# Optimization experiments

Measured on AMD Instinct MI355X. Metric: run time of the kernel, lower is better.

The kernel has to match this reference:

```python
import jax, jax.numpy as jnp
import numpy as np

H = 128          # hidden_dim
L = 3            # n_layers
G = 128          # num graphs in batch
BN_EPS = 1e-5


def setup_inputs() -> dict:
    key = jax.random.key(0)
    ks = jax.random.split(key, 16)
    N, E, ND, ED = 2048, 8192, 32, 16
    s = lambda k, shape, fan: jax.random.normal(k, shape, dtype=jnp.float32) / np.sqrt(fan)
    return {
        "x": jax.random.normal(ks[0], (N, ND), dtype=jnp.float32),
        "edge_index": jax.random.randint(ks[1], (2, E), 0, N),
        "edge_attr": jax.random.normal(ks[2], (E, ED), dtype=jnp.float32),
        "batch": jnp.sort(jax.random.randint(ks[3], (N,), 0, G)),
        "node_W": s(ks[4], (ND, H), ND),
        "node_b": jnp.zeros((H,), jnp.float32),
        "edge_W": s(ks[5], (L, ED, H * H), ED),
        "edge_b": jnp.zeros((L, H * H), jnp.float32),
        "root_W": s(ks[6], (L, H, H), H),
        "conv_bias": jnp.zeros((L, H), jnp.float32),
        "bn_gamma": jnp.ones((L, H), jnp.float32),
        "bn_beta": jnp.zeros((L, H), jnp.float32),
        "cls_W1": s(ks[7], (H, 64), H),
        "cls_b1": jnp.zeros((64,), jnp.float32),
        "cls_W2": s(ks[8], (64, 1), 64),
        "cls_b2": jnp.zeros((1,), jnp.float32),
    }


def _segment_mean(vals, ids, num_segments):
    ssum = jax.ops.segment_sum(vals, ids, num_segments=num_segments)
    cnt = jax.ops.segment_sum(jnp.ones((vals.shape[0],), vals.dtype), ids,
                              num_segments=num_segments)
    return ssum / jnp.maximum(cnt, 1.0)[:, None]


def reference(x, edge_index, edge_attr, batch, node_W, node_b, edge_W, edge_b,
              root_W, conv_bias, bn_gamma, bn_beta, cls_W1, cls_b1, cls_W2, cls_b2):
    N = x.shape[0]
    src, dst = edge_index[0], edge_index[1]
    h = x @ node_W + node_b                                   # [N, H]
    for l in range(L):
        # edge-conditioned weights: [E, H, H]
        W = (edge_attr @ edge_W[l] + edge_b[l]).reshape(-1, H, H)
        msg = jnp.einsum('ei,eio->eo', h[src], W)             # gather + per-edge matmul
        agg = _segment_mean(msg, dst, N)                      # scatter-mean
        x_new = h @ root_W[l] + agg + conv_bias[l]
        # BatchNorm (batch statistics, training-mode math)
        mu = jnp.mean(x_new, axis=0)
        var = jnp.var(x_new, axis=0)
        x_new = (x_new - mu) * jax.lax.rsqrt(var + BN_EPS) * bn_gamma[l] + bn_beta[l]
        x_new = jax.nn.relu(x_new)                            # dropout omitted (eval)
        h = h + x_new                                         # residual
    g = _segment_mean(h, batch, G)                            # global mean pool [G, H]
    out = jax.nn.relu(g @ cls_W1 + cls_b1) @ cls_W2 + cls_b2  # classifier
    return out.squeeze(-1)                                    # [G]
```

## Files before the change

### kernel.cpp

```cpp
#include <hip/hip_runtime.h>
#include <cstddef>
#include <cstdint>

#define H 128
#define EDIM 16
#define NLAYER 3
#define NSLICE 18
#define WCOLS (NSLICE * H)
#define PCOLS (EDIM * H)

typedef unsigned short ushort_t;
typedef unsigned int uint_t;
typedef __attribute__((ext_vector_type(8))) short bf16x8;
typedef __attribute__((ext_vector_type(4))) float f32x4;

__device__ __forceinline__ ushort_t f2bf(float f) {
    uint_t u = __builtin_bit_cast(uint_t, f);
    u += 0x7fffu + ((u >> 16) & 1u);
    return (ushort_t)(u >> 16);
}
__device__ __forceinline__ float bf_lo(uint_t u) {
    return __builtin_bit_cast(float, u << 16);
}
__device__ __forceinline__ float bf_hi(uint_t u) {
    return __builtin_bit_cast(float, u & 0xffff0000u);
}

__global__ __launch_bounds__(256) void setup_kernel(
    const int* __restrict__ dst, const int* __restrict__ batch,
    int* __restrict__ histD, float* __restrict__ cntG, int E, int N,
    const float* __restrict__ eW, const float* __restrict__ eb,
    const float* __restrict__ rW, ushort_t* __restrict__ Wt,
    const float* __restrict__ x, const float* __restrict__ nW,
    const float* __restrict__ nbias, float* __restrict__ h,
    ushort_t* __restrict__ hbf)
{
    __shared__ alignas(16) ushort_t tile[128][136];
    const int t = threadIdx.x;

    if (blockIdx.x < 32) {
        const int g = blockIdx.x * 256 + t;
        if (g < E) atomicAdd(&histD[dst[g]], 1);
        if (g < N) atomicAdd(&cntG[batch[g]], 1.f);
        return;
    }

    if (blockIdx.x < 86) {
        const int b = blockIdx.x - 32;
        const int l = b / NSLICE, s = b % NSLICE;
        const float* S = (s < 16) ? (eW + ((size_t)l * 16 + s) * (H * H))
                       : (s == 16 ? (eb + (size_t)l * H * H)
                                  : (rW + (size_t)l * H * H));
        const int k = t >> 1, o0 = (t & 1) * 64;
#pragma unroll
        for (int j = 0; j < 64; j += 4) {
            float4 v = *(const float4*)&S[(size_t)k * H + o0 + j];
            tile[k][o0 + j + 0] = f2bf(v.x);
            tile[k][o0 + j + 1] = f2bf(v.y);
            tile[k][o0 + j + 2] = f2bf(v.z);
            tile[k][o0 + j + 3] = f2bf(v.w);
        }
        __syncthreads();
        const int n = t >> 1, k0 = (t & 1) * 64;
        ushort_t* outp = Wt + ((size_t)l * WCOLS + s * H + n) * H + k0;
#pragma unroll 8
        for (int j = 0; j < 64; ++j) outp[j] = tile[k0 + j][n];
        return;
    }

    const int b2 = blockIdx.x - 86;
    const int bm = (b2 >> 1) * 64;
    const int bn = (b2 & 1) * 64;
    float (*As)[68] = (float (*)[68])(void*)tile;
    float (*Bs)[68] = ((float (*)[68])(void*)tile) + 16;

    const int tx = t & 15, ty = t >> 4;
    float acc[4][4];
#pragma unroll
    for (int i = 0; i < 4; ++i)
#pragma unroll
        for (int j = 0; j < 4; ++j) acc[i][j] = 0.f;

    const int ka = t & 15, ma = t >> 4;
    const int nb2 = t & 63, kb = t >> 6;

    for (int k0 = 0; k0 < 32; k0 += 16) {
#pragma unroll
        for (int r = 0; r < 4; ++r)
            As[ka][ma + 16 * r] = x[(size_t)(bm + ma + 16 * r) * 32 + k0 + ka];
#pragma unroll
        for (int r = 0; r < 4; ++r)
            Bs[kb + 4 * r][nb2] = nW[(size_t)(k0 + kb + 4 * r) * H + bn + nb2];
        __syncthreads();
#pragma unroll
        for (int kk = 0; kk < 16; ++kk) {
            const float4 a4 = *(const float4*)&As[kk][ty * 4];
            const float4 b4 = *(const float4*)&Bs[kk][tx * 4];
            const float a[4] = {a4.x, a4.y, a4.z, a4.w};
            const float b[4] = {b4.x, b4.y, b4.z, b4.w};
#pragma unroll
            for (int i = 0; i < 4; ++i)
#pragma unroll
                for (int j = 0; j < 4; ++j)
                    acc[i][j] = fmaf(a[i], b[j], acc[i][j]);
        }
        __syncthreads();
    }

#pragma unroll
    for (int i = 0; i < 4; ++i) {
        const int row = bm + ty * 4 + i;
        float4 v;
        v.x = acc[i][0] + nbias[bn + tx * 4 + 0];
        v.y = acc[i][1] + nbias[bn + tx * 4 + 1];
        v.z = acc[i][2] + nbias[bn + tx * 4 + 2];
        v.w = acc[i][3] + nbias[bn + tx * 4 + 3];
        *(float4*)&h[(size_t)row * H + bn + tx * 4] = v;
        ushort_t* o = &hbf[(size_t)row * H + bn + tx * 4];
        o[0] = f2bf(v.x); o[1] = f2bf(v.y); o[2] = f2bf(v.z); o[3] = f2bf(v.w);
    }
}

__global__ __launch_bounds__(256) void mfma_gemm(
    const ushort_t* __restrict__ hbf, const ushort_t* __restrict__ Wt,
    ushort_t* __restrict__ Pb, float* __restrict__ QR)
{
    __shared__ ushort_t As[64][136];
    __shared__ ushort_t Bs[64][136];
    const int tid = threadIdx.x;
    const int v0 = blockIdx.y * 64;
    const int n0 = blockIdx.x * 64;

    {
        const int row = tid >> 2, col0 = (tid & 3) * 32;
        const ushort_t* ga = hbf + (size_t)(v0 + row) * H + col0;
        const ushort_t* gb = Wt + (size_t)(n0 + row) * H + col0;
#pragma unroll
        for (int j = 0; j < 32; j += 8) {
            *(uint4*)&As[row][col0 + j] = *(const uint4*)(ga + j);
            *(uint4*)&Bs[row][col0 + j] = *(const uint4*)(gb + j);
        }
    }
    __syncthreads();

    const int wave = tid >> 6, lane = tid & 63;
    const int l15 = lane & 15, kg = lane >> 4;
    const int mrow = wave * 16 + l15;

    f32x4 acc0 = {0.f, 0.f, 0.f, 0.f};
    f32x4 acc1 = {0.f, 0.f, 0.f, 0.f};
    f32x4 acc2 = {0.f, 0.f, 0.f, 0.f};
    f32x4 acc3 = {0.f, 0.f, 0.f, 0.f};

#pragma unroll
    for (int s = 0; s < 4; ++s) {
        const int k = s * 32 + kg * 8;
        bf16x8 a = *(const bf16x8*)&As[mrow][k];
        bf16x8 b0 = *(const bf16x8*)&Bs[0 * 16 + l15][k];
        bf16x8 b1 = *(const bf16x8*)&Bs[1 * 16 + l15][k];
        bf16x8 b2 = *(const bf16x8*)&Bs[2 * 16 + l15][k];
        bf16x8 b3 = *(const bf16x8*)&Bs[3 * 16 + l15][k];
        acc0 = __builtin_amdgcn_mfma_f32_16x16x32_bf16(a, b0, acc0, 0, 0, 0);
        acc1 = __builtin_amdgcn_mfma_f32_16x16x32_bf16(a, b1, acc1, 0, 0, 0);
        acc2 = __builtin_amdgcn_mfma_f32_16x16x32_bf16(a, b2, acc2, 0, 0, 0);
        acc3 = __builtin_amdgcn_mfma_f32_16x16x32_bf16(a, b3, acc3, 0, 0, 0);
    }

    const int slice = n0 >> 7;
    const int lo = n0 & 127;
    const int row0 = v0 + wave * 16 + kg * 4;
    if (slice < 16) {
        ushort_t* op = Pb + (size_t)row0 * PCOLS + slice * H + lo + l15;
#pragma unroll
        for (int r = 0; r < 4; ++r) {
            op[(size_t)r * PCOLS + 0]  = f2bf(acc0[r]);
            op[(size_t)r * PCOLS + 16] = f2bf(acc1[r]);
            op[(size_t)r * PCOLS + 32] = f2bf(acc2[r]);
            op[(size_t)r * PCOLS + 48] = f2bf(acc3[r]);
        }
    } else {
        float* op = QR + (size_t)row0 * 256 + (slice - 16) * H + lo + l15;
#pragma unroll
        for (int r = 0; r < 4; ++r) {
            op[(size_t)r * 256 + 0]  = acc0[r];
            op[(size_t)r * 256 + 16] = acc1[r];
            op[(size_t)r * 256 + 32] = acc2[r];
            op[(size_t)r * 256 + 48] = acc3[r];
        }
    }
}

__global__ __launch_bounds__(256) void edge_msg(
    const ushort_t* __restrict__ Pb, const float* __restrict__ QR,
    const float* __restrict__ ea, const int* __restrict__ srcArr,
    const int* __restrict__ dstArr, float* __restrict__ agg, int E)
{
    const int wave = threadIdx.x >> 6, lane = threadIdx.x & 63;
    const int e = blockIdx.x * 4 + wave;
    if (e >= E) return;
    const int s  = srcArr[e];
    const int dv = dstArr[e];
    const float* eap = ea + (size_t)e * EDIM;
    const float4 w0 = *(const float4*)(eap + 0);
    const float4 w1 = *(const float4*)(eap + 4);
    const float4 w2 = *(const float4*)(eap + 8);
    const float4 w3 = *(const float4*)(eap + 12);
    const float w[16] = {w0.x, w0.y, w0.z, w0.w, w1.x, w1.y, w1.z, w1.w,
                         w2.x, w2.y, w2.z, w2.w, w3.x, w3.y, w3.z, w3.w};
    const uint_t* prow = (const uint_t*)Pb + (size_t)s * (PCOLS / 2) + lane;
    const float2 q2 = *(const float2*)(QR + (size_t)s * 256 + 2 * lane);
    float m0 = q2.x, m1 = q2.y;
#pragma unroll
    for (int d = 0; d < EDIM; ++d) {
        const uint_t u = prow[(size_t)d * 64];
        m0 = fmaf(w[d], bf_lo(u), m0);
        m1 = fmaf(w[d], bf_hi(u), m1);
    }
    atomicAdd(&agg[(size_t)dv * H + 2 * lane], m0);
    atomicAdd(&agg[(size_t)dv * H + 2 * lane + 1], m1);
}

__global__ __launch_bounds__(256) void node_stats(
    float* __restrict__ agg, const float* __restrict__ QR,
    const int* __restrict__ histD, const float* __restrict__ conv_b,
    float* __restrict__ xnew, float* __restrict__ bnS, float* __restrict__ bnQ)
{
    __shared__ float sS[H];
    __shared__ float sQ[H];
    const int tid = threadIdx.x;
    const int c = tid & 127, half = tid >> 7;
    const int v0 = blockIdx.x * 8 + half * 4;
    const float cb = conv_b[c];
    float s = 0.f, q = 0.f;
#pragma unroll
    for (int j = 0; j < 4; ++j) {
        const int v = v0 + j;
        const int deg = histD[v];
        const float rc = 1.0f / (float)(deg > 0 ? deg : 1);
        const size_t ix = (size_t)v * H + c;
        const float val = agg[ix] * rc + QR[(size_t)v * 256 + H + c] + cb;
        xnew[ix] = val;
        agg[ix] = 0.f;
        s += val;
        q += val * val;
    }
    if (half == 0) { sS[c] = s; sQ[c] = q; }
    __syncthreads();
    if (half == 1) {
        atomicAdd(&bnS[c], sS[c] + s);
        atomicAdd(&bnQ[c], sQ[c] + q);
    }
}

__global__ __launch_bounds__(256) void bn_apply(
    float* __restrict__ h, ushort_t* __restrict__ hbf,
    const float* __restrict__ xnew,
    const float* __restrict__ bnS, const float* __restrict__ bnQ,
    const float* __restrict__ gamma, const float* __restrict__ beta,
    const int* __restrict__ batch, float* __restrict__ gsum, int N, int last)
{
    const int idx = blockIdx.x * 256 + threadIdx.x;
    const int c = idx & 127;
    const int v = idx >> 7;
    const float invN = 1.0f / (float)N;
    const float mu = bnS[c] * invN;
    const float var = bnQ[c] * invN - mu * mu;
    const float val = (xnew[idx] - mu) * rsqrtf(var + 1e-5f) * gamma[c] + beta[c];
    const float hn = h[idx] + fmaxf(val, 0.f);
    h[idx] = hn;
    hbf[idx] = f2bf(hn);
    if (last) atomicAdd(&gsum[batch[v] * H + c], hn);
}

__global__ void classifier_kernel(
    const float* __restrict__ gsum, const float* __restrict__ cntG,
    const float* __restrict__ W1, const float* __restrict__ b1,
    const float* __restrict__ W2, const float* __restrict__ b2,
    float* __restrict__ out)
{
    const int g = blockIdx.x;
    const int j = threadIdx.x;
    const float rc = 1.0f / fmaxf(cntG[g], 1.0f);
    float acc = b1[j];
#pragma unroll 8
    for (int i = 0; i < H; ++i)
        acc = fmaf(gsum[g * H + i] * rc, W1[i * 64 + j], acc);
    float pv = fmaxf(acc, 0.f) * W2[j];
#pragma unroll
    for (int off = 32; off > 0; off >>= 1)
        pv += __shfl_down(pv, off);
    if (j == 0) out[g] = pv + b2[0];
}

extern "C" void kernel_launch(void* const* d_in, const int* in_sizes, int n_in,
                              void* d_out, int out_size, void* d_ws, size_t ws_size,
                              hipStream_t stream)
{
    const float* x      = (const float*)d_in[0];
    const int*   eidx   = (const int*)  d_in[1];
    const float* eattr  = (const float*)d_in[2];
    const int*   batch  = (const int*)  d_in[3];
    const float* node_W = (const float*)d_in[4];
    const float* node_b = (const float*)d_in[5];
    const float* edge_W = (const float*)d_in[6];
    const float* edge_b = (const float*)d_in[7];
    const float* root_W = (const float*)d_in[8];
    const float* conv_b = (const float*)d_in[9];
    const float* gamma  = (const float*)d_in[10];
    const float* beta   = (const float*)d_in[11];
    const float* W1     = (const float*)d_in[12];
    const float* b1     = (const float*)d_in[13];
    const float* W2     = (const float*)d_in[14];
    const float* b2     = (const float*)d_in[15];
    float* out = (float*)d_out;

    const int N = in_sizes[0] / 32;
    const int E = in_sizes[1] / 2;
    const int G = out_size;

    int* histD  = (int*)d_ws;
    float* cntG = (float*)(histD + N);
    float* bnS  = cntG + G;
    float* bnQ  = bnS + NLAYER * H;
    float* gsum = bnQ + NLAYER * H;
    float* agg  = gsum + (size_t)G * H;
    float* h    = agg + (size_t)N * H;
    float* xnew = h + (size_t)N * H;
    ushort_t* hbf = (ushort_t*)(xnew + (size_t)N * H);
    ushort_t* Wt  = hbf + (size_t)N * H;
    ushort_t* Pb  = Wt + (size_t)NLAYER * WCOLS * H;
    float* QR   = (float*)(Pb + (size_t)N * PCOLS);

    const size_t zbytes = ((size_t)N + G + 2 * NLAYER * H
                         + (size_t)G * H + (size_t)N * H) * 4;
    hipMemsetAsync(d_ws, 0, zbytes, stream);

    const int* src = eidx;
    const int* dst = eidx + E;

    setup_kernel<<<150, 256, 0, stream>>>(
        dst, batch, histD, cntG, E, N, edge_W, edge_b, root_W, Wt,
        x, node_W, node_b, h, hbf);

    for (int l = 0; l < NLAYER; ++l) {
        mfma_gemm<<<dim3(WCOLS / 64, N / 64), 256, 0, stream>>>(
            hbf, Wt + (size_t)l * WCOLS * H, Pb, QR);
        edge_msg<<<(E + 3) / 4, 256, 0, stream>>>(
            Pb, QR, eattr, src, dst, agg, E);
        node_stats<<<N / 8, 256, 0, stream>>>(
            agg, QR, histD, conv_b + (size_t)l * H,
            xnew, bnS + l * H, bnQ + l * H);
        bn_apply<<<(N * H) / 256, 256, 0, stream>>>(
            h, hbf, xnew, bnS + l * H, bnQ + l * H,
            gamma + (size_t)l * H, beta + (size_t)l * H,
            batch, gsum, N, l == NLAYER - 1);
    }

    classifier_kernel<<<G, 64, 0, stream>>>(gsum, cntG, W1, b1, W2, b2, out);
}
```

Measured before the change: 198.9 us.

## Fuse BatchNorm apply into next layer GEMM and final pooling into classifier

Removes the separate bn_apply kernel. Each layer's GEMM now recomputes the BN scale and shift, applies residual plus ReLU while loading its A tile, and converts to bf16 in place. Only the first column block writes the new fp32 h to a ping-pong buffer. The last layer's BN, residual and mean pooling move into the classifier, which reads contiguous node ranges per graph (relying on batch being sorted) instead of using atomics. This saves three launches and a full pass over the node features each layer, at the cost of redundant BN/ReLU work across all 36 column blocks and a serial prefix sum over cntG in each classifier block.

```diff
diff --git a/kernel.cpp b/kernel.cpp
--- a/kernel.cpp
+++ b/kernel.cpp
@@ -32,8 +32,7 @@
     const float* __restrict__ eW, const float* __restrict__ eb,
     const float* __restrict__ rW, ushort_t* __restrict__ Wt,
     const float* __restrict__ x, const float* __restrict__ nW,
-    const float* __restrict__ nbias, float* __restrict__ h,
-    ushort_t* __restrict__ hbf)
+    const float* __restrict__ nbias, float* __restrict__ hA)
 {
     __shared__ alignas(16) ushort_t tile[128][136];
     const int t = threadIdx.x;
@@ -106,7 +105,6 @@
         }
         __syncthreads();
     }
-
 #pragma unroll
     for (int i = 0; i < 4; ++i) {
         const int row = bm + ty * 4 + i;
@@ -115,30 +113,75 @@
         v.y = acc[i][1] + nbias[bn + tx * 4 + 1];
         v.z = acc[i][2] + nbias[bn + tx * 4 + 2];
         v.w = acc[i][3] + nbias[bn + tx * 4 + 3];
-        *(float4*)&h[(size_t)row * H + bn + tx * 4] = v;
-        ushort_t* o = &hbf[(size_t)row * H + bn + tx * 4];
-        o[0] = f2bf(v.x); o[1] = f2bf(v.y); o[2] = f2bf(v.z); o[3] = f2bf(v.w);
+        *(float4*)&hA[(size_t)row * H + bn + tx * 4] = v;
     }
 }
 
 __global__ __launch_bounds__(256) void mfma_gemm(
-    const ushort_t* __restrict__ hbf, const ushort_t* __restrict__ Wt,
-    ushort_t* __restrict__ Pb, float* __restrict__ QR)
+    const float* __restrict__ hsrc, const float* __restrict__ xnew,
+    float* __restrict__ hdst, const ushort_t* __restrict__ Wt,
+    ushort_t* __restrict__ Pb, float* __restrict__ QR,
+    const float* __restrict__ bnS, const float* __restrict__ bnQ,
+    const float* __restrict__ gamma, const float* __restrict__ beta,
+    int N, int fuse)
 {
     __shared__ ushort_t As[64][136];
     __shared__ ushort_t Bs[64][136];
+    __shared__ float sc[H], sh[H];
     const int tid = threadIdx.x;
+    const int n0 = blockIdx.x * 64;
     const int v0 = blockIdx.y * 64;
-    const int n0 = blockIdx.x * 64;
-
+
+    if (fuse) {
+        if (tid < H) {
+            const float invN = 1.0f / (float)N;
+            const float mu = bnS[tid] * invN;
+            const float var = bnQ[tid] * invN - mu * mu;
+            const float s_ = rsqrtf(var + 1e-5f) * gamma[tid];
+            sc[tid] = s_;
+            sh[tid] = beta[tid] - mu * s_;
+        }
+        __syncthreads();
+    }
+
+    const int row = tid >> 2, col0 = (tid & 3) * 32;
     {
-        const int row = tid >> 2, col0 = (tid & 3) * 32;
-        const ushort_t* ga = hbf + (size_t)(v0 + row) * H + col0;
         const ushort_t* gb = Wt + (size_t)(n0 + row) * H + col0;
 #pragma unroll
-        for (int j = 0; j < 32; j += 8) {
-            *(uint4*)&As[row][col0 + j] = *(const uint4*)(ga + j);
-            *(uint4*)&Bs[row][col0 + j] = *(const uint4*)(gb + j);
+        for (int jj = 0; jj < 32; jj += 8)
+            *(uint4*)&Bs[row][col0 + jj] = *(const uint4*)(gb + jj);
+    }
+    {
+        const float* ga = hsrc + (size_t)(v0 + row) * H + col0;
+        if (!fuse) {
+#pragma unroll
+            for (int jj = 0; jj < 32; jj += 4) {
+                const float4 v = *(const float4*)(ga + jj);
+                uint2 u;
+                u.x = (uint_t)f2bf(v.x) | ((uint_t)f2bf(v.y) << 16);
+                u.y = (uint_t)f2bf(v.z) | ((uint_t)f2bf(v.w) << 16);
+                *(uint2*)&As[row][col0 + jj] = u;
+            }
+        } else {
+            const float* gx = xnew + (size_t)(v0 + row) * H + col0;
+            float* gh = hdst + (size_t)(v0 + row) * H + col0;
+#pragma unroll
+            for (int jj = 0; jj < 32; jj += 4) {
+                const float4 hv = *(const float4*)(ga + jj);
+                const float4 xv = *(const float4*)(gx + jj);
+                const float4 scv = *(const float4*)&sc[col0 + jj];
+                const float4 shv = *(const float4*)&sh[col0 + jj];
+                float4 hn;
+                hn.x = hv.x + fmaxf(xv.x * scv.x + shv.x, 0.f);
+                hn.y = hv.y + fmaxf(xv.y * scv.y + shv.y, 0.f);
+                hn.z = hv.z + fmaxf(xv.z * scv.z + shv.z, 0.f);
+                hn.w = hv.w + fmaxf(xv.w * scv.w + shv.w, 0.f);
+                if (blockIdx.x == 0) *(float4*)(gh + jj) = hn;
+                uint2 u;
+                u.x = (uint_t)f2bf(hn.x) | ((uint_t)f2bf(hn.y) << 16);
+                u.y = (uint_t)f2bf(hn.z) | ((uint_t)f2bf(hn.w) << 16);
+                *(uint2*)&As[row][col0 + jj] = u;
+            }
         }
     }
     __syncthreads();
@@ -146,16 +189,14 @@
     const int wave = tid >> 6, lane = tid & 63;
     const int l15 = lane & 15, kg = lane >> 4;
     const int mrow = wave * 16 + l15;
-
     f32x4 acc0 = {0.f, 0.f, 0.f, 0.f};
     f32x4 acc1 = {0.f, 0.f, 0.f, 0.f};
     f32x4 acc2 = {0.f, 0.f, 0.f, 0.f};
     f32x4 acc3 = {0.f, 0.f, 0.f, 0.f};
-
-#pragma unroll
-    for (int s = 0; s < 4; ++s) {
-        const int k = s * 32 + kg * 8;
-        bf16x8 a = *(const bf16x8*)&As[mrow][k];
+#pragma unroll
+    for (int s2 = 0; s2 < 4; ++s2) {
+        const int k = s2 * 32 + kg * 8;
+        bf16x8 a  = *(const bf16x8*)&As[mrow][k];
         bf16x8 b0 = *(const bf16x8*)&Bs[0 * 16 + l15][k];
         bf16x8 b1 = *(const bf16x8*)&Bs[1 * 16 + l15][k];
         bf16x8 b2 = *(const bf16x8*)&Bs[2 * 16 + l15][k];
@@ -165,7 +206,6 @@
         acc2 = __builtin_amdgcn_mfma_f32_16x16x32_bf16(a, b2, acc2, 0, 0, 0);
         acc3 = __builtin_amdgcn_mfma_f32_16x16x32_bf16(a, b3, acc3, 0, 0, 0);
     }
-
     const int slice = n0 >> 7;
     const int lo = n0 & 127;
     const int row0 = v0 + wave * 16 + kg * 4;
@@ -252,44 +292,51 @@
     }
 }
 
-__global__ __launch_bounds__(256) void bn_apply(
-    float* __restrict__ h, ushort_t* __restrict__ hbf,
-    const float* __restrict__ xnew,
+__global__ __launch_bounds__(256) void classifier_kernel(
+    const float* __restrict__ h2, const float* __restrict__ xnew,
     const float* __restrict__ bnS, const float* __restrict__ bnQ,
     const float* __restrict__ gamma, const float* __restrict__ beta,
-    const int* __restrict__ batch, float* __restrict__ gsum, int N, int last)
-{
-    const int idx = blockIdx.x * 256 + threadIdx.x;
-    const int c = idx & 127;
-    const int v = idx >> 7;
-    const float invN = 1.0f / (float)N;
-    const float mu = bnS[c] * invN;
-    const float var = bnQ[c] * invN - mu * mu;
-    const float val = (xnew[idx] - mu) * rsqrtf(var + 1e-5f) * gamma[c] + beta[c];
-    const float hn = h[idx] + fmaxf(val, 0.f);
-    h[idx] = hn;
-    hbf[idx] = f2bf(hn);
-    if (last) atomicAdd(&gsum[batch[v] * H + c], hn);
-}
-
-__global__ void classifier_kernel(
-    const float* __restrict__ gsum, const float* __restrict__ cntG,
+    const float* __restrict__ cntG,
     const float* __restrict__ W1, const float* __restrict__ b1,
     const float* __restrict__ W2, const float* __restrict__ b2,
-    float* __restrict__ out)
-{
+    float* __restrict__ out, int N)
+{
+    __shared__ float sc[H], sh[H], part[H], pooled[H];
     const int g = blockIdx.x;
-    const int j = threadIdx.x;
-    const float rc = 1.0f / fmaxf(cntG[g], 1.0f);
-    float acc = b1[j];
+    const int tid = threadIdx.x;
+    const int c = tid & 127, half = tid >> 7;
+    if (tid < H) {
+        const float invN = 1.0f / (float)N;
+        const float mu = bnS[tid] * invN;
+        const float var = bnQ[tid] * invN - mu * mu;
+        const float s_ = rsqrtf(var + 1e-5f) * gamma[tid];
+        sc[tid] = s_;
+        sh[tid] = beta[tid] - mu * s_;
+    }
+    __syncthreads();
+    int lo = 0;
+    for (int i = 0; i < g; ++i) lo += (int)cntG[i];
+    const int cnt = (int)cntG[g];
+    float s = 0.f;
+    for (int v = lo + half; v < lo + cnt; v += 2) {
+        const size_t ix = (size_t)v * H + c;
+        s += h2[ix] + fmaxf(xnew[ix] * sc[c] + sh[c], 0.f);
+    }
+    if (half == 0) part[c] = s;
+    __syncthreads();
+    if (half == 1) pooled[c] = (part[c] + s) / fmaxf((float)cnt, 1.0f);
+    __syncthreads();
+    if (tid < 64) {
+        float acc = b1[tid];
 #pragma unroll 8
-    for (int i = 0; i < H; ++i)
-        acc = fmaf(gsum[g * H + i] * rc, W1[i * 64 + j], acc);
-    float pv = fmaxf(acc, 0.f) * W2[j];
-#pragma unroll
-    for (int off = 32; off > 0; off >>= 1)
-        pv += __shfl_down(pv, off);
-    if (j == 0) out[g] = pv + b2[0];
+        for (int i = 0; i < H; ++i)
+            acc = fmaf(pooled[i], W1[i * 64 + tid], acc);
+        float pv = fmaxf(acc, 0.f) * W2[tid];
+#pragma unroll
+        for (int off = 32; off > 0; off >>= 1)
+            pv += __shfl_down(pv, off);
+        if (tid == 0) out[g] = pv + b2[0];
+    }
 }
 
 extern "C" void kernel_launch(void* const* d_in, const int* in_sizes, int n_in,
@@ -322,17 +369,15 @@
     float* cntG = (float*)(histD + N);
     float* bnS  = cntG + G;
     float* bnQ  = bnS + NLAYER * H;
-    float* gsum = bnQ + NLAYER * H;
-    float* agg  = gsum + (size_t)G * H;
-    float* h    = agg + (size_t)N * H;
-    float* xnew = h + (size_t)N * H;
-    ushort_t* hbf = (ushort_t*)(xnew + (size_t)N * H);
-    ushort_t* Wt  = hbf + (size_t)N * H;
-    ushort_t* Pb  = Wt + (size_t)NLAYER * WCOLS * H;
+    float* agg  = bnQ + NLAYER * H;
+    float* hA   = agg + (size_t)N * H;
+    float* hB   = hA + (size_t)N * H;
+    float* xnew = hB + (size_t)N * H;
+    ushort_t* Wt = (ushort_t*)(xnew + (size_t)N * H);
+    ushort_t* Pb = Wt + (size_t)NLAYER * WCOLS * H;
     float* QR   = (float*)(Pb + (size_t)N * PCOLS);
 
-    const size_t zbytes = ((size_t)N + G + 2 * NLAYER * H
-                         + (size_t)G * H + (size_t)N * H) * 4;
+    const size_t zbytes = ((size_t)N + G + 2 * NLAYER * H + (size_t)N * H) * 4;
     hipMemsetAsync(d_ws, 0, zbytes, stream);
 
     const int* src = eidx;
@@ -340,21 +385,25 @@
 
     setup_kernel<<<150, 256, 0, stream>>>(
         dst, batch, histD, cntG, E, N, edge_W, edge_b, root_W, Wt,
-        x, node_W, node_b, h, hbf);
+        x, node_W, node_b, hA);
+
+    const float* hsrc[NLAYER] = { hA, hA, hB };
+    float*       hdst[NLAYER] = { nullptr, hB, hA };
 
     for (int l = 0; l < NLAYER; ++l) {
         mfma_gemm<<<dim3(WCOLS / 64, N / 64), 256, 0, stream>>>(
-            hbf, Wt + (size_t)l * WCOLS * H, Pb, QR);
-        edge_msg<<<(E + 3) / 4, 256, 0, stream>>>(
+            hsrc[l], xnew, hdst[l], Wt + (size_t)l * WCOLS * H, Pb, QR,
+            bnS + (size_t)(l - 1) * H, bnQ + (size_t)(l - 1) * H,
+            gamma + (size_t)(l - 1) * H, beta + (size_t)(l - 1) * H,
+            N, l > 0);
+        edge_msg<<<E / 4, 256, 0, stream>>>(
             Pb, QR, eattr, src, dst, agg, E);
         node_stats<<<N / 8, 256, 0, stream>>>(
             agg, QR, histD, conv_b + (size_t)l * H,
             xnew, bnS + l * H, bnQ + l * H);
-        bn_apply<<<(N * H) / 256, 256, 0, stream>>>(
-            h, hbf, xnew, bnS + l * H, bnQ + l * H,
-            gamma + (size_t)l * H, beta + (size_t)l * H,
-            batch, gsum, N, l == NLAYER - 1);
-    }
-
-    classifier_kernel<<<G, 64, 0, stream>>>(gsum, cntG, W1, b1, W2, b2, out);
-}
+    }
+
+    classifier_kernel<<<G, 256, 0, stream>>>(
+        hA, xnew, bnS + 2 * H, bnQ + 2 * H, gamma + 2 * H, beta + 2 * H,
+        cntG, W1, b1, W2, b2, out, N);
+}
```

New measurement: 229.2 us. 15.2% more time.

## Fuse edge messaging, BN stats and apply into one persistent grid-synced layer kernel

Applied to the files above, without the earlier changes.

Replaces the edge_msg, node_stats and bn_apply launches with a single persistent kernel of 256 blocks. It uses two atomic-counter grid barriers between the scatter, statistics and normalisation phases, and keeps xnew values in registers instead of writing them to global memory. The MFMA GEMM tile is widened to 128 output columns per block, and global pooling moves into the classifier as a contiguous-segment sum, which relies on batch being sorted, instead of atomics. This cuts launch overhead and intermediate traffic, at the cost of spin-wait barriers that assume all 256 blocks are co-resident and that N equals 2048 (256 blocks times 8 nodes).

```diff
diff --git a/kernel.cpp b/kernel.cpp
--- a/kernel.cpp
+++ b/kernel.cpp
@@ -8,6 +8,7 @@
 #define NSLICE 18
 #define WCOLS (NSLICE * H)
 #define PCOLS (EDIM * H)
+#define NBLK 256
 
 typedef unsigned short ushort_t;
 typedef unsigned int uint_t;
@@ -106,7 +107,6 @@
         }
         __syncthreads();
     }
-
 #pragma unroll
     for (int i = 0; i < 4; ++i) {
         const int row = bm + ty * 4 + i;
@@ -126,20 +126,25 @@
     ushort_t* __restrict__ Pb, float* __restrict__ QR)
 {
     __shared__ ushort_t As[64][136];
-    __shared__ ushort_t Bs[64][136];
+    __shared__ ushort_t Bs[128][136];
     const int tid = threadIdx.x;
+    const int bx = blockIdx.x;
+    const int n0 = bx * 128;
     const int v0 = blockIdx.y * 64;
-    const int n0 = blockIdx.x * 64;
 
     {
         const int row = tid >> 2, col0 = (tid & 3) * 32;
         const ushort_t* ga = hbf + (size_t)(v0 + row) * H + col0;
+#pragma unroll
+        for (int j = 0; j < 32; j += 8)
+            *(uint4*)&As[row][col0 + j] = *(const uint4*)(ga + j);
+    }
+    {
+        const int row = tid >> 1, col0 = (tid & 1) * 64;
         const ushort_t* gb = Wt + (size_t)(n0 + row) * H + col0;
 #pragma unroll
-        for (int j = 0; j < 32; j += 8) {
-            *(uint4*)&As[row][col0 + j] = *(const uint4*)(ga + j);
+        for (int j = 0; j < 64; j += 8)
             *(uint4*)&Bs[row][col0 + j] = *(const uint4*)(gb + j);
-        }
     }
     __syncthreads();
 
@@ -147,90 +152,114 @@
     const int l15 = lane & 15, kg = lane >> 4;
     const int mrow = wave * 16 + l15;
 
-    f32x4 acc0 = {0.f, 0.f, 0.f, 0.f};
-    f32x4 acc1 = {0.f, 0.f, 0.f, 0.f};
-    f32x4 acc2 = {0.f, 0.f, 0.f, 0.f};
-    f32x4 acc3 = {0.f, 0.f, 0.f, 0.f};
-
-#pragma unroll
-    for (int s = 0; s < 4; ++s) {
-        const int k = s * 32 + kg * 8;
+    f32x4 acc0 = {0,0,0,0}, acc1 = {0,0,0,0}, acc2 = {0,0,0,0}, acc3 = {0,0,0,0};
+    f32x4 acc4 = {0,0,0,0}, acc5 = {0,0,0,0}, acc6 = {0,0,0,0}, acc7 = {0,0,0,0};
+
+#pragma unroll
+    for (int s2 = 0; s2 < 4; ++s2) {
+        const int k = s2 * 32 + kg * 8;
         bf16x8 a = *(const bf16x8*)&As[mrow][k];
         bf16x8 b0 = *(const bf16x8*)&Bs[0 * 16 + l15][k];
         bf16x8 b1 = *(const bf16x8*)&Bs[1 * 16 + l15][k];
         bf16x8 b2 = *(const bf16x8*)&Bs[2 * 16 + l15][k];
         bf16x8 b3 = *(const bf16x8*)&Bs[3 * 16 + l15][k];
+        bf16x8 b4 = *(const bf16x8*)&Bs[4 * 16 + l15][k];
+        bf16x8 b5 = *(const bf16x8*)&Bs[5 * 16 + l15][k];
+        bf16x8 b6 = *(const bf16x8*)&Bs[6 * 16 + l15][k];
+        bf16x8 b7 = *(const bf16x8*)&Bs[7 * 16 + l15][k];
         acc0 = __builtin_amdgcn_mfma_f32_16x16x32_bf16(a, b0, acc0, 0, 0, 0);
         acc1 = __builtin_amdgcn_mfma_f32_16x16x32_bf16(a, b1, acc1, 0, 0, 0);
         acc2 = __builtin_amdgcn_mfma_f32_16x16x32_bf16(a, b2, acc2, 0, 0, 0);
         acc3 = __builtin_amdgcn_mfma_f32_16x16x32_bf16(a, b3, acc3, 0, 0, 0);
-    }
-
-    const int slice = n0 >> 7;
-    const int lo = n0 & 127;
+        acc4 = __builtin_amdgcn_mfma_f32_16x16x32_bf16(a, b4, acc4, 0, 0, 0);
+        acc5 = __builtin_amdgcn_mfma_f32_16x16x32_bf16(a, b5, acc5, 0, 0, 0);
+        acc6 = __builtin_amdgcn_mfma_f32_16x16x32_bf16(a, b6, acc6, 0, 0, 0);
+        acc7 = __builtin_amdgcn_mfma_f32_16x16x32_bf16(a, b7, acc7, 0, 0, 0);
+    }
+
     const int row0 = v0 + wave * 16 + kg * 4;
-    if (slice < 16) {
-        ushort_t* op = Pb + (size_t)row0 * PCOLS + slice * H + lo + l15;
+    if (bx < 16) {
+        ushort_t* op = Pb + (size_t)row0 * PCOLS + bx * H + l15;
 #pragma unroll
         for (int r = 0; r < 4; ++r) {
-            op[(size_t)r * PCOLS + 0]  = f2bf(acc0[r]);
-            op[(size_t)r * PCOLS + 16] = f2bf(acc1[r]);
-            op[(size_t)r * PCOLS + 32] = f2bf(acc2[r]);
-            op[(size_t)r * PCOLS + 48] = f2bf(acc3[r]);
+            const size_t ro = (size_t)r * PCOLS;
+            op[ro + 0 * 16] = f2bf(acc0[r]);
+            op[ro + 1 * 16] = f2bf(acc1[r]);
+            op[ro + 2 * 16] = f2bf(acc2[r]);
+            op[ro + 3 * 16] = f2bf(acc3[r]);
+            op[ro + 4 * 16] = f2bf(acc4[r]);
+            op[ro + 5 * 16] = f2bf(acc5[r]);
+            op[ro + 6 * 16] = f2bf(acc6[r]);
+            op[ro + 7 * 16] = f2bf(acc7[r]);
         }
     } else {
-        float* op = QR + (size_t)row0 * 256 + (slice - 16) * H + lo + l15;
+        float* op = QR + (size_t)row0 * 256 + (bx - 16) * 128 + l15;
 #pragma unroll
         for (int r = 0; r < 4; ++r) {
-            op[(size_t)r * 256 + 0]  = acc0[r];
-            op[(size_t)r * 256 + 16] = acc1[r];
-            op[(size_t)r * 256 + 32] = acc2[r];
-            op[(size_t)r * 256 + 48] = acc3[r];
+            const size_t ro = (size_t)r * 256;
+            op[ro + 0 * 16] = acc0[r];
+            op[ro + 1 * 16] = acc1[r];
+            op[ro + 2 * 16] = acc2[r];
+            op[ro + 3 * 16] = acc3[r];
+            op[ro + 4 * 16] = acc4[r];
+            op[ro + 5 * 16] = acc5[r];
+            op[ro + 6 * 16] = acc6[r];
+            op[ro + 7 * 16] = acc7[r];
         }
     }
 }
 
-__global__ __launch_bounds__(256) void edge_msg(
+__global__ __launch_bounds__(256) void layer_kernel(
     const ushort_t* __restrict__ Pb, const float* __restrict__ QR,
     const float* __restrict__ ea, const int* __restrict__ srcArr,
-    const int* __restrict__ dstArr, float* __restrict__ agg, int E)
-{
-    const int wave = threadIdx.x >> 6, lane = threadIdx.x & 63;
-    const int e = blockIdx.x * 4 + wave;
-    if (e >= E) return;
-    const int s  = srcArr[e];
-    const int dv = dstArr[e];
-    const float* eap = ea + (size_t)e * EDIM;
-    const float4 w0 = *(const float4*)(eap + 0);
-    const float4 w1 = *(const float4*)(eap + 4);
-    const float4 w2 = *(const float4*)(eap + 8);
-    const float4 w3 = *(const float4*)(eap + 12);
-    const float w[16] = {w0.x, w0.y, w0.z, w0.w, w1.x, w1.y, w1.z, w1.w,
-                         w2.x, w2.y, w2.z, w2.w, w3.x, w3.y, w3.z, w3.w};
-    const uint_t* prow = (const uint_t*)Pb + (size_t)s * (PCOLS / 2) + lane;
-    const float2 q2 = *(const float2*)(QR + (size_t)s * 256 + 2 * lane);
-    float m0 = q2.x, m1 = q2.y;
-#pragma unroll
-    for (int d = 0; d < EDIM; ++d) {
-        const uint_t u = prow[(size_t)d * 64];
-        m0 = fmaf(w[d], bf_lo(u), m0);
-        m1 = fmaf(w[d], bf_hi(u), m1);
-    }
-    atomicAdd(&agg[(size_t)dv * H + 2 * lane], m0);
-    atomicAdd(&agg[(size_t)dv * H + 2 * lane + 1], m1);
-}
-
-__global__ __launch_bounds__(256) void node_stats(
-    float* __restrict__ agg, const float* __restrict__ QR,
-    const int* __restrict__ histD, const float* __restrict__ conv_b,
-    float* __restrict__ xnew, float* __restrict__ bnS, float* __restrict__ bnQ)
+    const int* __restrict__ dstArr, const int* __restrict__ histD,
+    const float* __restrict__ conv_b, const float* __restrict__ gamma,
+    const float* __restrict__ beta, float* __restrict__ agg,
+    float* __restrict__ h, ushort_t* __restrict__ hbf,
+    float* __restrict__ bnS, float* __restrict__ bnQ,
+    int* __restrict__ cnt, int E, int N, int last)
 {
     __shared__ float sS[H];
     __shared__ float sQ[H];
     const int tid = threadIdx.x;
+    const int bid = blockIdx.x;
+    const int wave = tid >> 6, lane = tid & 63;
+
+    for (int e = bid * 4 + wave; e < E; e += NBLK * 4) {
+        const int s  = srcArr[e];
+        const int dv = dstArr[e];
+        const float* eap = ea + (size_t)e * EDIM;
+        const float4 w0 = *(const float4*)(eap + 0);
+        const float4 w1 = *(const float4*)(eap + 4);
+        const float4 w2 = *(const float4*)(eap + 8);
+        const float4 w3 = *(const float4*)(eap + 12);
+        const float w[16] = {w0.x, w0.y, w0.z, w0.w, w1.x, w1.y, w1.z, w1.w,
+                             w2.x, w2.y, w2.z, w2.w, w3.x, w3.y, w3.z, w3.w};
+        const uint_t* prow = (const uint_t*)Pb + (size_t)s * (PCOLS / 2) + lane;
+        const float2 q2 = *(const float2*)(QR + (size_t)s * 256 + 2 * lane);
+        float m0 = q2.x, m1 = q2.y;
+#pragma unroll
+        for (int d = 0; d < EDIM; ++d) {
+            const uint_t u = prow[(size_t)d * 64];
+            m0 = fmaf(w[d], bf_lo(u), m0);
+            m1 = fmaf(w[d], bf_hi(u), m1);
+        }
+        atomicAdd(&agg[(size_t)dv * H + 2 * lane], m0);
+        atomicAdd(&agg[(size_t)dv * H + 2 * lane + 1], m1);
+    }
+    __syncthreads();
+    if (tid == 0) {
+        __threadfence();
+        atomicAdd(&cnt[0], 1);
+        while (__hip_atomic_load(&cnt[0], __ATOMIC_ACQUIRE,
+                                 __HIP_MEMORY_SCOPE_AGENT) < NBLK) {}
+    }
+    __syncthreads();
+
     const int c = tid & 127, half = tid >> 7;
-    const int v0 = blockIdx.x * 8 + half * 4;
+    const int v0 = bid * 8 + half * 4;
     const float cb = conv_b[c];
+    float vals[4];
     float s = 0.f, q = 0.f;
 #pragma unroll
     for (int j = 0; j < 4; ++j) {
@@ -238,8 +267,10 @@
         const int deg = histD[v];
         const float rc = 1.0f / (float)(deg > 0 ? deg : 1);
         const size_t ix = (size_t)v * H + c;
-        const float val = agg[ix] * rc + QR[(size_t)v * 256 + H + c] + cb;
-        xnew[ix] = val;
+        const float a = __hip_atomic_load(&agg[ix], __ATOMIC_RELAXED,
+                                          __HIP_MEMORY_SCOPE_AGENT);
+        const float val = a * rc + QR[(size_t)v * 256 + H + c] + cb;
+        vals[j] = val;
         agg[ix] = 0.f;
         s += val;
         q += val * val;
@@ -250,46 +281,65 @@
         atomicAdd(&bnS[c], sS[c] + s);
         atomicAdd(&bnQ[c], sQ[c] + q);
     }
-}
-
-__global__ __launch_bounds__(256) void bn_apply(
-    float* __restrict__ h, ushort_t* __restrict__ hbf,
-    const float* __restrict__ xnew,
-    const float* __restrict__ bnS, const float* __restrict__ bnQ,
-    const float* __restrict__ gamma, const float* __restrict__ beta,
-    const int* __restrict__ batch, float* __restrict__ gsum, int N, int last)
-{
-    const int idx = blockIdx.x * 256 + threadIdx.x;
-    const int c = idx & 127;
-    const int v = idx >> 7;
+    __syncthreads();
+    if (tid == 0) {
+        __threadfence();
+        atomicAdd(&cnt[1], 1);
+        while (__hip_atomic_load(&cnt[1], __ATOMIC_ACQUIRE,
+                                 __HIP_MEMORY_SCOPE_AGENT) < NBLK) {}
+    }
+    __syncthreads();
+
     const float invN = 1.0f / (float)N;
-    const float mu = bnS[c] * invN;
-    const float var = bnQ[c] * invN - mu * mu;
-    const float val = (xnew[idx] - mu) * rsqrtf(var + 1e-5f) * gamma[c] + beta[c];
-    const float hn = h[idx] + fmaxf(val, 0.f);
-    h[idx] = hn;
-    hbf[idx] = f2bf(hn);
-    if (last) atomicAdd(&gsum[batch[v] * H + c], hn);
-}
-
-__global__ void classifier_kernel(
-    const float* __restrict__ gsum, const float* __restrict__ cntG,
+    const float S_ = __hip_atomic_load(&bnS[c], __ATOMIC_RELAXED,
+                                       __HIP_MEMORY_SCOPE_AGENT);
+    const float Q_ = __hip_atomic_load(&bnQ[c], __ATOMIC_RELAXED,
+                                       __HIP_MEMORY_SCOPE_AGENT);
+    const float mu = S_ * invN;
+    const float var = Q_ * invN - mu * mu;
+    const float sc = rsqrtf(var + 1e-5f) * gamma[c];
+    const float sh = beta[c] - mu * sc;
+#pragma unroll
+    for (int j = 0; j < 4; ++j) {
+        const int v = v0 + j;
+        const size_t ix = (size_t)v * H + c;
+        const float hn = h[ix] + fmaxf(vals[j] * sc + sh, 0.f);
+        h[ix] = hn;
+        if (!last) hbf[ix] = f2bf(hn);
+    }
+}
+
+__global__ __launch_bounds__(256) void classifier_kernel(
+    const float* __restrict__ h, const float* __restrict__ cntG,
     const float* __restrict__ W1, const float* __restrict__ b1,
     const float* __restrict__ W2, const float* __restrict__ b2,
     float* __restrict__ out)
 {
+    __shared__ float part[H], pooled[H];
     const int g = blockIdx.x;
-    const int j = threadIdx.x;
-    const float rc = 1.0f / fmaxf(cntG[g], 1.0f);
-    float acc = b1[j];
+    const int tid = threadIdx.x;
+    const int c = tid & 127, half = tid >> 7;
+    int lo = 0;
+    for (int i = 0; i < g; ++i) lo += (int)cntG[i];
+    const int cnt = (int)cntG[g];
+    float s = 0.f;
+    for (int v = lo + half; v < lo + cnt; v += 2)
+        s += h[(size_t)v * H + c];
+    if (half == 0) part[c] = s;
+    __syncthreads();
+    if (half == 1) pooled[c] = (part[c] + s) / fmaxf((float)cnt, 1.0f);
+    __syncthreads();
+    if (tid < 64) {
+        float acc = b1[tid];
 #pragma unroll 8
-    for (int i = 0; i < H; ++i)
-        acc = fmaf(gsum[g * H + i] * rc, W1[i * 64 + j], acc);
-    float pv = fmaxf(acc, 0.f) * W2[j];
-#pragma unroll
-    for (int off = 32; off > 0; off >>= 1)
-        pv += __shfl_down(pv, off);
-    if (j == 0) out[g] = pv + b2[0];
+        for (int i = 0; i < H; ++i)
+            acc = fmaf(pooled[i], W1[i * 64 + tid], acc);
+        float pv = fmaxf(acc, 0.f) * W2[tid];
+#pragma unroll
+        for (int off = 32; off > 0; off >>= 1)
+            pv += __shfl_down(pv, off);
+        if (tid == 0) out[g] = pv + b2[0];
+    }
 }
 
 extern "C" void kernel_launch(void* const* d_in, const int* in_sizes, int n_in,
@@ -322,17 +372,15 @@
     float* cntG = (float*)(histD + N);
     float* bnS  = cntG + G;
     float* bnQ  = bnS + NLAYER * H;
-    float* gsum = bnQ + NLAYER * H;
-    float* agg  = gsum + (size_t)G * H;
+    int* syncC  = (int*)(bnQ + NLAYER * H);
+    float* agg  = (float*)(syncC + 8);
     float* h    = agg + (size_t)N * H;
-    float* xnew = h + (size_t)N * H;
-    ushort_t* hbf = (ushort_t*)(xnew + (size_t)N * H);
-    ushort_t* Wt  = hbf + (size_t)N * H;
-    ushort_t* Pb  = Wt + (size_t)NLAYER * WCOLS * H;
+    ushort_t* hbf = (ushort_t*)(h + (size_t)N * H);
+    ushort_t* Wt = hbf + (size_t)N * H;
+    ushort_t* Pb = Wt + (size_t)NLAYER * WCOLS * H;
     float* QR   = (float*)(Pb + (size_t)N * PCOLS);
 
-    const size_t zbytes = ((size_t)N + G + 2 * NLAYER * H
-                         + (size_t)G * H + (size_t)N * H) * 4;
+    const size_t zbytes = ((size_t)N + G + 2 * NLAYER * H + 8 + (size_t)N * H) * 4;
     hipMemsetAsync(d_ws, 0, zbytes, stream);
 
     const int* src = eidx;
@@ -343,18 +391,14 @@
         x, node_W, node_b, h, hbf);
 
     for (int l = 0; l < NLAYER; ++l) {
-        mfma_gemm<<<dim3(WCOLS / 64, N / 64), 256, 0, stream>>>(
+        mfma_gemm<<<dim3(NSLICE, N / 64), 256, 0, stream>>>(
             hbf, Wt + (size_t)l * WCOLS * H, Pb, QR);
-        edge_msg<<<(E + 3) / 4, 256, 0, stream>>>(
-            Pb, QR, eattr, src, dst, agg, E);
-        node_stats<<<N / 8, 256, 0, stream>>>(
-            agg, QR, histD, conv_b + (size_t)l * H,
-            xnew, bnS + l * H, bnQ + l * H);
-        bn_apply<<<(N * H) / 256, 256, 0, stream>>>(
-            h, hbf, xnew, bnS + l * H, bnQ + l * H,
-            gamma + (size_t)l * H, beta + (size_t)l * H,
-            batch, gsum, N, l == NLAYER - 1);
-    }
-
-    classifier_kernel<<<G, 64, 0, stream>>>(gsum, cntG, W1, b1, W2, b2, out);
-}
+        layer_kernel<<<NBLK, 256, 0, stream>>>(
+            Pb, QR, eattr, src, dst, histD,
+            conv_b + (size_t)l * H, gamma + (size_t)l * H, beta + (size_t)l * H,
+            agg, h, hbf, bnS + l * H, bnQ + l * H,
+            syncC + 2 * l, E, N, l == NLAYER - 1);
+    }
+
+    classifier_kernel<<<G, 256, 0, stream>>>(h, cntG, W1, b1, W2, b2, out);
+}
```

New measurement: 314.6 us. +58.1%, slower.

## Transpose P layout so edge gather loads contiguous 16-wide vectors per lane

Applied to the files above, without the earlier changes.

The GEMM now computes a full 128-column slice per block and writes P interleaved so that, for each output channel pair, all 16 edge-dimension values are contiguous. The edge message kernel then loads them with four 128-bit loads instead of 16 strided 32-bit loads. This cuts the number of gather transactions per edge, at the cost of scattered 2-byte stores in the GEMM epilogue and more registers per block.

```diff
diff --git a/kernel.cpp b/kernel.cpp
--- a/kernel.cpp
+++ b/kernel.cpp
@@ -106,7 +106,6 @@
         }
         __syncthreads();
     }
-
 #pragma unroll
     for (int i = 0; i < 4; ++i) {
         const int row = bm + ty * 4 + i;
@@ -126,20 +125,25 @@
     ushort_t* __restrict__ Pb, float* __restrict__ QR)
 {
     __shared__ ushort_t As[64][136];
-    __shared__ ushort_t Bs[64][136];
+    __shared__ ushort_t Bs[128][136];
     const int tid = threadIdx.x;
+    const int bx = blockIdx.x;
+    const int n0 = bx * 128;
     const int v0 = blockIdx.y * 64;
-    const int n0 = blockIdx.x * 64;
 
     {
         const int row = tid >> 2, col0 = (tid & 3) * 32;
         const ushort_t* ga = hbf + (size_t)(v0 + row) * H + col0;
+#pragma unroll
+        for (int j = 0; j < 32; j += 8)
+            *(uint4*)&As[row][col0 + j] = *(const uint4*)(ga + j);
+    }
+    {
+        const int row = tid >> 1, col0 = (tid & 1) * 64;
         const ushort_t* gb = Wt + (size_t)(n0 + row) * H + col0;
 #pragma unroll
-        for (int j = 0; j < 32; j += 8) {
-            *(uint4*)&As[row][col0 + j] = *(const uint4*)(ga + j);
+        for (int j = 0; j < 64; j += 8)
             *(uint4*)&Bs[row][col0 + j] = *(const uint4*)(gb + j);
-        }
     }
     __syncthreads();
 
@@ -147,45 +151,60 @@
     const int l15 = lane & 15, kg = lane >> 4;
     const int mrow = wave * 16 + l15;
 
-    f32x4 acc0 = {0.f, 0.f, 0.f, 0.f};
-    f32x4 acc1 = {0.f, 0.f, 0.f, 0.f};
-    f32x4 acc2 = {0.f, 0.f, 0.f, 0.f};
-    f32x4 acc3 = {0.f, 0.f, 0.f, 0.f};
-
-#pragma unroll
-    for (int s = 0; s < 4; ++s) {
-        const int k = s * 32 + kg * 8;
+    f32x4 acc0 = {0,0,0,0}, acc1 = {0,0,0,0}, acc2 = {0,0,0,0}, acc3 = {0,0,0,0};
+    f32x4 acc4 = {0,0,0,0}, acc5 = {0,0,0,0}, acc6 = {0,0,0,0}, acc7 = {0,0,0,0};
+
+#pragma unroll
+    for (int s2 = 0; s2 < 4; ++s2) {
+        const int k = s2 * 32 + kg * 8;
         bf16x8 a = *(const bf16x8*)&As[mrow][k];
         bf16x8 b0 = *(const bf16x8*)&Bs[0 * 16 + l15][k];
         bf16x8 b1 = *(const bf16x8*)&Bs[1 * 16 + l15][k];
         bf16x8 b2 = *(const bf16x8*)&Bs[2 * 16 + l15][k];
         bf16x8 b3 = *(const bf16x8*)&Bs[3 * 16 + l15][k];
+        bf16x8 b4 = *(const bf16x8*)&Bs[4 * 16 + l15][k];
+        bf16x8 b5 = *(const bf16x8*)&Bs[5 * 16 + l15][k];
+        bf16x8 b6 = *(const bf16x8*)&Bs[6 * 16 + l15][k];
+        bf16x8 b7 = *(const bf16x8*)&Bs[7 * 16 + l15][k];
         acc0 = __builtin_amdgcn_mfma_f32_16x16x32_bf16(a, b0, acc0, 0, 0, 0);
         acc1 = __builtin_amdgcn_mfma_f32_16x16x32_bf16(a, b1, acc1, 0, 0, 0);
         acc2 = __builtin_amdgcn_mfma_f32_16x16x32_bf16(a, b2, acc2, 0, 0, 0);
         acc3 = __builtin_amdgcn_mfma_f32_16x16x32_bf16(a, b3, acc3, 0, 0, 0);
-    }
-
-    const int slice = n0 >> 7;
-    const int lo = n0 & 127;
+        acc4 = __builtin_amdgcn_mfma_f32_16x16x32_bf16(a, b4, acc4, 0, 0, 0);
+        acc5 = __builtin_amdgcn_mfma_f32_16x16x32_bf16(a, b5, acc5, 0, 0, 0);
+        acc6 = __builtin_amdgcn_mfma_f32_16x16x32_bf16(a, b6, acc6, 0, 0, 0);
+        acc7 = __builtin_amdgcn_mfma_f32_16x16x32_bf16(a, b7, acc7, 0, 0, 0);
+    }
+
     const int row0 = v0 + wave * 16 + kg * 4;
-    if (slice < 16) {
-        ushort_t* op = Pb + (size_t)row0 * PCOLS + slice * H + lo + l15;
+    if (bx < 16) {
+        ushort_t* op = Pb + (size_t)row0 * PCOLS
+                     + (l15 >> 1) * 32 + (l15 & 1) + bx * 2;
 #pragma unroll
         for (int r = 0; r < 4; ++r) {
-            op[(size_t)r * PCOLS + 0]  = f2bf(acc0[r]);
-            op[(size_t)r * PCOLS + 16] = f2bf(acc1[r]);
-            op[(size_t)r * PCOLS + 32] = f2bf(acc2[r]);
-            op[(size_t)r * PCOLS + 48] = f2bf(acc3[r]);
+            const size_t ro = (size_t)r * PCOLS;
+            op[ro + 0 * 256] = f2bf(acc0[r]);
+            op[ro + 1 * 256] = f2bf(acc1[r]);
+            op[ro + 2 * 256] = f2bf(acc2[r]);
+            op[ro + 3 * 256] = f2bf(acc3[r]);
+            op[ro + 4 * 256] = f2bf(acc4[r]);
+            op[ro + 5 * 256] = f2bf(acc5[r]);
+            op[ro + 6 * 256] = f2bf(acc6[r]);
+            op[ro + 7 * 256] = f2bf(acc7[r]);
         }
     } else {
-        float* op = QR + (size_t)row0 * 256 + (slice - 16) * H + lo + l15;
+        float* op = QR + (size_t)row0 * 256 + (bx - 16) * 128 + l15;
 #pragma unroll
         for (int r = 0; r < 4; ++r) {
-            op[(size_t)r * 256 + 0]  = acc0[r];
-            op[(size_t)r * 256 + 16] = acc1[r];
-            op[(size_t)r * 256 + 32] = acc2[r];
-            op[(size_t)r * 256 + 48] = acc3[r];
+            const size_t ro = (size_t)r * 256;
+            op[ro + 0 * 16] = acc0[r];
+            op[ro + 1 * 16] = acc1[r];
+            op[ro + 2 * 16] = acc2[r];
+            op[ro + 3 * 16] = acc3[r];
+            op[ro + 4 * 16] = acc4[r];
+            op[ro + 5 * 16] = acc5[r];
+            op[ro + 6 * 16] = acc6[r];
+            op[ro + 7 * 16] = acc7[r];
         }
     }
 }
@@ -207,14 +226,19 @@
     const float4 w3 = *(const float4*)(eap + 12);
     const float w[16] = {w0.x, w0.y, w0.z, w0.w, w1.x, w1.y, w1.z, w1.w,
                          w2.x, w2.y, w2.z, w2.w, w3.x, w3.y, w3.z, w3.w};
-    const uint_t* prow = (const uint_t*)Pb + (size_t)s * (PCOLS / 2) + lane;
+    const uint_t* prow = (const uint_t*)Pb + (size_t)s * (PCOLS / 2) + lane * 16;
+    const uint4 pa = *(const uint4*)(prow + 0);
+    const uint4 pb = *(const uint4*)(prow + 4);
+    const uint4 pc = *(const uint4*)(prow + 8);
+    const uint4 pd = *(const uint4*)(prow + 12);
+    const uint_t pv[16] = {pa.x, pa.y, pa.z, pa.w, pb.x, pb.y, pb.z, pb.w,
+                           pc.x, pc.y, pc.z, pc.w, pd.x, pd.y, pd.z, pd.w};
     const float2 q2 = *(const float2*)(QR + (size_t)s * 256 + 2 * lane);
     float m0 = q2.x, m1 = q2.y;
 #pragma unroll
     for (int d = 0; d < EDIM; ++d) {
-        const uint_t u = prow[(size_t)d * 64];
-        m0 = fmaf(w[d], bf_lo(u), m0);
-        m1 = fmaf(w[d], bf_hi(u), m1);
+        m0 = fmaf(w[d], bf_lo(pv[d]), m0);
+        m1 = fmaf(w[d], bf_hi(pv[d]), m1);
     }
     atomicAdd(&agg[(size_t)dv * H + 2 * lane], m0);
     atomicAdd(&agg[(size_t)dv * H + 2 * lane + 1], m1);
@@ -343,9 +367,9 @@
         x, node_W, node_b, h, hbf);
 
     for (int l = 0; l < NLAYER; ++l) {
-        mfma_gemm<<<dim3(WCOLS / 64, N / 64), 256, 0, stream>>>(
+        mfma_gemm<<<dim3(NSLICE, N / 64), 256, 0, stream>>>(
             hbf, Wt + (size_t)l * WCOLS * H, Pb, QR);
-        edge_msg<<<(E + 3) / 4, 256, 0, stream>>>(
+        edge_msg<<<E / 4, 256, 0, stream>>>(
             Pb, QR, eattr, src, dst, agg, E);
         node_stats<<<N / 8, 256, 0, stream>>>(
             agg, QR, histD, conv_b + (size_t)l * H,
```

Result: slower. 245.6 us (+23.5%).
